# Optimization experiments

Measured on AMD Instinct MI355X. Metric: run time of the kernel, lower is better.

The kernel has to match this reference:

```python
import jax, jax.numpy as jnp
from jax import lax
import numpy as np

N = 131072      # sample_size (number of SDE paths)
T = 500         # number of time points -> T-1 Euler-Maruyama steps
H = 64          # hidden_size of the tiny drift/diffusion MLPs
MU = 0.1
SIGMA = 0.2


def _col_eye(h, scale):
    # emulates scale * eye(h, 1): only [0, 0] element is `scale`
    return jnp.zeros((h, 1), jnp.float32).at[0, 0].set(scale)


def _row_eye(h):
    # emulates eye(1, h): only [0, 0] element is 1
    return jnp.zeros((1, h), jnp.float32).at[0, 0].set(1.0)


def setup_inputs() -> dict:
    key = jax.random.key(0)
    k1, k2 = jax.random.split(key)
    # positive initial prices in [1.0, 1.5) so log(terminal/initial) stays finite
    initial_states = jax.random.uniform(k1, (N, 1), jnp.float32) * 0.5 + 1.0
    times = jnp.linspace(0.0, 1.0, T).astype(jnp.float32)
    # standard-normal draws; scaled by sqrt(dt) inside reference
    noise = jax.random.normal(k2, (T - 1, N, 1), jnp.float32)
    return {
        "initial_states": initial_states,
        "times": times,
        "noise": noise,
        "f1_w": _col_eye(H, MU), "f1_b": jnp.zeros((H,), jnp.float32),
        "f2_w": _row_eye(H),     "f2_b": jnp.zeros((1,), jnp.float32),
        "g1_w": _col_eye(H, SIGMA), "g1_b": jnp.zeros((H,), jnp.float32),
        "g2_w": _row_eye(H),        "g2_b": jnp.zeros((1,), jnp.float32),
    }


def _mlp(y, w1, b1, w2, b2):
    # y: (N, 1) -> (N, 1); tanh(Linear) -> tanh(Linear), as in DeepSDE.f / .g
    h = jnp.tanh(y @ w1.T + b1)          # (N, H)
    return jnp.tanh(h @ w2.T + b2)       # (N, 1)


def reference(initial_states, times, noise,
              f1_w, f1_b, f2_w, f2_b,
              g1_w, g1_b, g2_w, g2_b):
    dts = times[1:] - times[:-1]         # (T-1,)

    def step(y, inp):
        dt, z = inp                      # dt scalar, z (N, 1)
        dW = jnp.sqrt(dt) * z            # Brownian increment
        fv = _mlp(y, f1_w, f1_b, f2_w, f2_b)   # drift, (N, 1)
        gv = _mlp(y, g1_w, g1_b, g2_w, g2_b)   # diffusion (N,1,1) squeezed, brownian_size=1
        return y + fv * dt + gv * dW, None     # Euler-Maruyama (torchsde ito default)

    terminal_states, _ = lax.scan(step, initial_states, (dts, noise))
    return jnp.log(terminal_states / initial_states)  # estimated_log_returns (N, 1)
```

## Files before the change

### kernel.cpp

```cpp
#include <hip/hip_runtime.h>
#include <cstdint>

#define NPATH 131072
#define TPTS  500
#define NSTEP (TPTS - 1)
#define HID   64
#define BLOCK 256

#define K2LOG2E 2.8853900817779268f

__device__ __forceinline__ float fexp2(float x) { return __builtin_amdgcn_exp2f(x); }
__device__ __forceinline__ float frcp(float x)  { return __builtin_amdgcn_rcpf(x); }

__device__ __forceinline__ float sde_step(float y, float dt, float sdt, float z,
                                          float fw1, float fb1, float fw2, float fD,
                                          float gw1, float gb1, float gw2, float gD)
{
    float zdt = sdt * z;
    float ef  = fexp2(fmaf(fw1, y, fb1));
    float rf  = frcp(ef + 1.0f);
    float af  = fmaf(fw2, rf, fD);
    float r2f = frcp(fexp2(af) + 1.0f);
    float fv  = fmaf(-2.0f, r2f, 1.0f);
    float eg  = fexp2(fmaf(gw1, y, gb1));
    float rg  = frcp(eg + 1.0f);
    float ag  = fmaf(gw2, rg, gD);
    float r2g = frcp(fexp2(ag) + 1.0f);
    float gv  = fmaf(-2.0f, r2g, 1.0f);

    y = fmaf(fv, dt, y);
    return fmaf(gv, zdt, y);
}

__global__ __launch_bounds__(BLOCK) void deepsde_kernel(
    const float* __restrict__ y0,
    const float* __restrict__ times,
    const float* __restrict__ noise,
    const float* __restrict__ f1_w, const float* __restrict__ f1_b,
    const float* __restrict__ f2_w, const float* __restrict__ f2_b,
    const float* __restrict__ g1_w, const float* __restrict__ g1_b,
    const float* __restrict__ g2_w, const float* __restrict__ g2_b,
    float* __restrict__ out)
{
    __shared__ float2 s_dt[NSTEP];
    __shared__ float  s_w1p[2][HID], s_b1p[2][HID], s_w2t[2][HID];
    __shared__ float  s_D[2];
    __shared__ int    s_n[2];

    const int tid = threadIdx.x;

    for (int t = tid; t < NSTEP; t += BLOCK) {
        float dt = times[t + 1] - times[t];
        s_dt[t] = make_float2(dt, sqrtf(dt));
    }

    if (tid < 128) {
        const int which = tid >> 6;
        const int lane  = tid & 63;
        const float* w1 = which ? g1_w : f1_w;
        const float* b1 = which ? g1_b : f1_b;
        const float* w2 = which ? g2_w : f2_w;
        const float* b2 = which ? g2_b : f2_b;
        float w1v = w1[lane];
        float b1v = b1[lane];
        float w2v = w2[lane];
        bool active = (w1v != 0.0f);
        unsigned long long mask = __ballot(active);
        float csum = active ? 0.0f : w2v * tanhf(b1v);
        float asum = active ? w2v : 0.0f;
        for (int off = 32; off > 0; off >>= 1) {
            csum += __shfl_down(csum, off);
            asum += __shfl_down(asum, off);
        }
        if (lane == 0) {
            s_n[which] = __popcll(mask);
            s_D[which] = K2LOG2E * (csum + b2[0] + asum);
        }
        if (active) {
            int rank = __popcll(mask & ((1ull << lane) - 1ull));
            s_w1p[which][rank] = K2LOG2E * w1v;
            s_b1p[which][rank] = K2LOG2E * b1v;
            s_w2t[which][rank] = -2.0f * K2LOG2E * w2v;
        }
    }
    __syncthreads();

    const int i = blockIdx.x * BLOCK + tid;
    const int nf = s_n[0], ng = s_n[1];
    const float fD = s_D[0], gD = s_D[1];

    float y = y0[i];
    const float yinit = y;

    if (nf == 1 && ng == 1) {
        const float fw1 = s_w1p[0][0], fb1 = s_b1p[0][0], fw2 = s_w2t[0][0];
        const float gw1 = s_w1p[1][0], gb1 = s_b1p[1][0], gw2 = s_w2t[1][0];

        const float* np = noise + i;

        float z0 = np[0 * NPATH];
        float z1 = np[1 * NPATH];
        float z2 = np[2 * NPATH];
        float z3 = np[3 * NPATH];
        float z4 = np[4 * NPATH];
        float z5 = np[5 * NPATH];
        float z6 = np[6 * NPATH];
        float z7 = np[7 * NPATH];

        int t = 0;
        for (; t + 15 < NSTEP; t += 8) {
            const float* pp = np + (size_t)(t + 8) * NPATH;
            float n0 = pp[0 * NPATH];
            float n1 = pp[1 * NPATH];
            float n2 = pp[2 * NPATH];
            float n3 = pp[3 * NPATH];
            float n4 = pp[4 * NPATH];
            float n5 = pp[5 * NPATH];
            float n6 = pp[6 * NPATH];
            float n7 = pp[7 * NPATH];
            float2 d0 = s_dt[t],     d1 = s_dt[t + 1], d2 = s_dt[t + 2], d3 = s_dt[t + 3];
            float2 d4 = s_dt[t + 4], d5 = s_dt[t + 5], d6 = s_dt[t + 6], d7 = s_dt[t + 7];
            y = sde_step(y, d0.x, d0.y, z0, fw1, fb1, fw2, fD, gw1, gb1, gw2, gD);
            y = sde_step(y, d1.x, d1.y, z1, fw1, fb1, fw2, fD, gw1, gb1, gw2, gD);
            y = sde_step(y, d2.x, d2.y, z2, fw1, fb1, fw2, fD, gw1, gb1, gw2, gD);
            y = sde_step(y, d3.x, d3.y, z3, fw1, fb1, fw2, fD, gw1, gb1, gw2, gD);
            y = sde_step(y, d4.x, d4.y, z4, fw1, fb1, fw2, fD, gw1, gb1, gw2, gD);
            y = sde_step(y, d5.x, d5.y, z5, fw1, fb1, fw2, fD, gw1, gb1, gw2, gD);
            y = sde_step(y, d6.x, d6.y, z6, fw1, fb1, fw2, fD, gw1, gb1, gw2, gD);
            y = sde_step(y, d7.x, d7.y, z7, fw1, fb1, fw2, fD, gw1, gb1, gw2, gD);
            z0 = n0; z1 = n1; z2 = n2; z3 = n3;
            z4 = n4; z5 = n5; z6 = n6; z7 = n7;
        }
        {
            float2 d0 = s_dt[t],     d1 = s_dt[t + 1], d2 = s_dt[t + 2], d3 = s_dt[t + 3];
            float2 d4 = s_dt[t + 4], d5 = s_dt[t + 5], d6 = s_dt[t + 6], d7 = s_dt[t + 7];
            y = sde_step(y, d0.x, d0.y, z0, fw1, fb1, fw2, fD, gw1, gb1, gw2, gD);
            y = sde_step(y, d1.x, d1.y, z1, fw1, fb1, fw2, fD, gw1, gb1, gw2, gD);
            y = sde_step(y, d2.x, d2.y, z2, fw1, fb1, fw2, fD, gw1, gb1, gw2, gD);
            y = sde_step(y, d3.x, d3.y, z3, fw1, fb1, fw2, fD, gw1, gb1, gw2, gD);
            y = sde_step(y, d4.x, d4.y, z4, fw1, fb1, fw2, fD, gw1, gb1, gw2, gD);
            y = sde_step(y, d5.x, d5.y, z5, fw1, fb1, fw2, fD, gw1, gb1, gw2, gD);
            y = sde_step(y, d6.x, d6.y, z6, fw1, fb1, fw2, fD, gw1, gb1, gw2, gD);
            y = sde_step(y, d7.x, d7.y, z7, fw1, fb1, fw2, fD, gw1, gb1, gw2, gD);
        }
        for (t += 8; t < NSTEP; ++t) {
            float z = np[(size_t)t * NPATH];
            float2 d = s_dt[t];
            y = sde_step(y, d.x, d.y, z, fw1, fb1, fw2, fD, gw1, gb1, gw2, gD);
        }
    } else {
        for (int t = 0; t < NSTEP; ++t) {
            float z = noise[(size_t)t * NPATH + i];
            float2 d = s_dt[t];
            float af = fD;
            for (int k = 0; k < nf; ++k) {
                float e = fexp2(fmaf(s_w1p[0][k], y, s_b1p[0][k]));
                float r = frcp(e + 1.0f);
                af = fmaf(s_w2t[0][k], r, af);
            }
            float fv = fmaf(-2.0f, frcp(fexp2(af) + 1.0f), 1.0f);
            float ag = gD;
            for (int k = 0; k < ng; ++k) {
                float e = fexp2(fmaf(s_w1p[1][k], y, s_b1p[1][k]));
                float r = frcp(e + 1.0f);
                ag = fmaf(s_w2t[1][k], r, ag);
            }
            float gv = fmaf(-2.0f, frcp(fexp2(ag) + 1.0f), 1.0f);
            y = fmaf(fv, d.x, y);
            y = fmaf(gv, d.y * z, y);
        }
    }

    out[i] = logf(y / yinit);
}

extern "C" void kernel_launch(void* const* d_in, const int* in_sizes, int n_in,
                              void* d_out, int out_size, void* d_ws, size_t ws_size,
                              hipStream_t stream)
{
    const float* y0    = (const float*)d_in[0];
    const float* times = (const float*)d_in[1];
    const float* noise = (const float*)d_in[2];
    const float* f1_w  = (const float*)d_in[3];
    const float* f1_b  = (const float*)d_in[4];
    const float* f2_w  = (const float*)d_in[5];
    const float* f2_b  = (const float*)d_in[6];
    const float* g1_w  = (const float*)d_in[7];
    const float* g1_b  = (const float*)d_in[8];
    const float* g2_w  = (const float*)d_in[9];
    const float* g2_b  = (const float*)d_in[10];
    float* out = (float*)d_out;

    deepsde_kernel<<<NPATH / BLOCK, BLOCK, 0, stream>>>(
        y0, times, noise,
        f1_w, f1_b, f2_w, f2_b,
        g1_w, g1_b, g2_w, g2_b,
        out);
}
```

Before: 369.8 us.

## Split drift and diffusion MLPs across thread pairs with lane shuffle exchange

Each SDE path is now handled by two adjacent threads: one evaluates the drift MLP and the other the diffusion MLP, and they swap results with a cross-lane shuffle every step. Launching twice as many threads halves the serial transcendental chain per thread, which exposes more parallelism, and launch bounds now request higher occupancy. In exchange both threads load the same noise and dt values and run the same Euler update, and every step adds a shuffle. The kernel was latency-bound with only 512 blocks, so the extra threads are meant to fill the GPU better.

```diff
diff --git a/kernel.cpp b/kernel.cpp
--- a/kernel.cpp
+++ b/kernel.cpp
@@ -6,33 +6,35 @@
 #define NSTEP (TPTS - 1)
 #define HID   64
 #define BLOCK 256
+#define NTHREADS (2 * NPATH)
 
 #define K2LOG2E 2.8853900817779268f
 
 __device__ __forceinline__ float fexp2(float x) { return __builtin_amdgcn_exp2f(x); }
 __device__ __forceinline__ float frcp(float x)  { return __builtin_amdgcn_rcpf(x); }
 
-__device__ __forceinline__ float sde_step(float y, float dt, float sdt, float z,
-                                          float fw1, float fb1, float fw2, float fD,
-                                          float gw1, float gb1, float gw2, float gD)
-{
-    float zdt = sdt * z;
-    float ef  = fexp2(fmaf(fw1, y, fb1));
-    float rf  = frcp(ef + 1.0f);
-    float af  = fmaf(fw2, rf, fD);
-    float r2f = frcp(fexp2(af) + 1.0f);
-    float fv  = fmaf(-2.0f, r2f, 1.0f);
-    float eg  = fexp2(fmaf(gw1, y, gb1));
-    float rg  = frcp(eg + 1.0f);
-    float ag  = fmaf(gw2, rg, gD);
-    float r2g = frcp(fexp2(ag) + 1.0f);
-    float gv  = fmaf(-2.0f, r2g, 1.0f);
-
+__device__ __forceinline__ float mlp1(float y, float w1, float b1, float w2t, float D)
+{
+    float e  = fexp2(fmaf(w1, y, b1));
+    float r  = frcp(e + 1.0f);
+    float a  = fmaf(w2t, r, D);
+    float r2 = frcp(fexp2(a) + 1.0f);
+    return fmaf(-2.0f, r2, 1.0f);
+}
+
+__device__ __forceinline__ float step2(float y, float dt, float sdt, float z, bool role,
+                                       float w1, float b1, float w2t, float D)
+{
+    float zdt    = sdt * z;
+    float mine   = mlp1(y, w1, b1, w2t, D);
+    float theirs = __shfl_xor(mine, 1, 64);
+    float fv = role ? theirs : mine;
+    float gv = role ? mine   : theirs;
     y = fmaf(fv, dt, y);
     return fmaf(gv, zdt, y);
 }
 
-__global__ __launch_bounds__(BLOCK) void deepsde_kernel(
+__global__ __launch_bounds__(BLOCK, 4) void deepsde_kernel(
     const float* __restrict__ y0,
     const float* __restrict__ times,
     const float* __restrict__ noise,
@@ -85,18 +87,22 @@
     }
     __syncthreads();
 
-    const int i = blockIdx.x * BLOCK + tid;
-    const int nf = s_n[0], ng = s_n[1];
-    const float fD = s_D[0], gD = s_D[1];
-
-    float y = y0[i];
+    const bool role = tid & 1;
+    const int  p    = blockIdx.x * (BLOCK / 2) + (tid >> 1);
+    const int  nf = s_n[0], ng = s_n[1];
+
+    float y = y0[p];
     const float yinit = y;
 
     if (nf == 1 && ng == 1) {
-        const float fw1 = s_w1p[0][0], fb1 = s_b1p[0][0], fw2 = s_w2t[0][0];
-        const float gw1 = s_w1p[1][0], gb1 = s_b1p[1][0], gw2 = s_w2t[1][0];
-
-        const float* np = noise + i;
+        const float fw1 = s_w1p[0][0], fb1 = s_b1p[0][0], fw2 = s_w2t[0][0], fDv = s_D[0];
+        const float gw1 = s_w1p[1][0], gb1 = s_b1p[1][0], gw2 = s_w2t[1][0], gDv = s_D[1];
+        const float w1  = role ? gw1 : fw1;
+        const float b1  = role ? gb1 : fb1;
+        const float w2t = role ? gw2 : fw2;
+        const float D   = role ? gDv : fDv;
+
+        const float* np = noise + p;
 
         float z0 = np[0 * NPATH];
         float z1 = np[1 * NPATH];
@@ -120,58 +126,61 @@
             float n7 = pp[7 * NPATH];
             float2 d0 = s_dt[t],     d1 = s_dt[t + 1], d2 = s_dt[t + 2], d3 = s_dt[t + 3];
             float2 d4 = s_dt[t + 4], d5 = s_dt[t + 5], d6 = s_dt[t + 6], d7 = s_dt[t + 7];
-            y = sde_step(y, d0.x, d0.y, z0, fw1, fb1, fw2, fD, gw1, gb1, gw2, gD);
-            y = sde_step(y, d1.x, d1.y, z1, fw1, fb1, fw2, fD, gw1, gb1, gw2, gD);
-            y = sde_step(y, d2.x, d2.y, z2, fw1, fb1, fw2, fD, gw1, gb1, gw2, gD);
-            y = sde_step(y, d3.x, d3.y, z3, fw1, fb1, fw2, fD, gw1, gb1, gw2, gD);
-            y = sde_step(y, d4.x, d4.y, z4, fw1, fb1, fw2, fD, gw1, gb1, gw2, gD);
-            y = sde_step(y, d5.x, d5.y, z5, fw1, fb1, fw2, fD, gw1, gb1, gw2, gD);
-            y = sde_step(y, d6.x, d6.y, z6, fw1, fb1, fw2, fD, gw1, gb1, gw2, gD);
-            y = sde_step(y, d7.x, d7.y, z7, fw1, fb1, fw2, fD, gw1, gb1, gw2, gD);
+            y = step2(y, d0.x, d0.y, z0, role, w1, b1, w2t, D);
+            y = step2(y, d1.x, d1.y, z1, role, w1, b1, w2t, D);
+            y = step2(y, d2.x, d2.y, z2, role, w1, b1, w2t, D);
+            y = step2(y, d3.x, d3.y, z3, role, w1, b1, w2t, D);
+            y = step2(y, d4.x, d4.y, z4, role, w1, b1, w2t, D);
+            y = step2(y, d5.x, d5.y, z5, role, w1, b1, w2t, D);
+            y = step2(y, d6.x, d6.y, z6, role, w1, b1, w2t, D);
+            y = step2(y, d7.x, d7.y, z7, role, w1, b1, w2t, D);
             z0 = n0; z1 = n1; z2 = n2; z3 = n3;
             z4 = n4; z5 = n5; z6 = n6; z7 = n7;
         }
         {
             float2 d0 = s_dt[t],     d1 = s_dt[t + 1], d2 = s_dt[t + 2], d3 = s_dt[t + 3];
             float2 d4 = s_dt[t + 4], d5 = s_dt[t + 5], d6 = s_dt[t + 6], d7 = s_dt[t + 7];
-            y = sde_step(y, d0.x, d0.y, z0, fw1, fb1, fw2, fD, gw1, gb1, gw2, gD);
-            y = sde_step(y, d1.x, d1.y, z1, fw1, fb1, fw2, fD, gw1, gb1, gw2, gD);
-            y = sde_step(y, d2.x, d2.y, z2, fw1, fb1, fw2, fD, gw1, gb1, gw2, gD);
-            y = sde_step(y, d3.x, d3.y, z3, fw1, fb1, fw2, fD, gw1, gb1, gw2, gD);
-            y = sde_step(y, d4.x, d4.y, z4, fw1, fb1, fw2, fD, gw1, gb1, gw2, gD);
-            y = sde_step(y, d5.x, d5.y, z5, fw1, fb1, fw2, fD, gw1, gb1, gw2, gD);
-            y = sde_step(y, d6.x, d6.y, z6, fw1, fb1, fw2, fD, gw1, gb1, gw2, gD);
-            y = sde_step(y, d7.x, d7.y, z7, fw1, fb1, fw2, fD, gw1, gb1, gw2, gD);
+            y = step2(y, d0.x, d0.y, z0, role, w1, b1, w2t, D);
+            y = step2(y, d1.x, d1.y, z1, role, w1, b1, w2t, D);
+            y = step2(y, d2.x, d2.y, z2, role, w1, b1, w2t, D);
+            y = step2(y, d3.x, d3.y, z3, role, w1, b1, w2t, D);
+            y = step2(y, d4.x, d4.y, z4, role, w1, b1, w2t, D);
+            y = step2(y, d5.x, d5.y, z5, role, w1, b1, w2t, D);
+            y = step2(y, d6.x, d6.y, z6, role, w1, b1, w2t, D);
+            y = step2(y, d7.x, d7.y, z7, role, w1, b1, w2t, D);
         }
         for (t += 8; t < NSTEP; ++t) {
             float z = np[(size_t)t * NPATH];
             float2 d = s_dt[t];
-            y = sde_step(y, d.x, d.y, z, fw1, fb1, fw2, fD, gw1, gb1, gw2, gD);
+            y = step2(y, d.x, d.y, z, role, w1, b1, w2t, D);
         }
     } else {
-        for (int t = 0; t < NSTEP; ++t) {
-            float z = noise[(size_t)t * NPATH + i];
-            float2 d = s_dt[t];
-            float af = fD;
-            for (int k = 0; k < nf; ++k) {
-                float e = fexp2(fmaf(s_w1p[0][k], y, s_b1p[0][k]));
-                float r = frcp(e + 1.0f);
-                af = fmaf(s_w2t[0][k], r, af);
+        if (!role) {
+            const float fD = s_D[0], gD = s_D[1];
+            for (int t = 0; t < NSTEP; ++t) {
+                float z = noise[(size_t)t * NPATH + p];
+                float2 d = s_dt[t];
+                float af = fD;
+                for (int k = 0; k < nf; ++k) {
+                    float e = fexp2(fmaf(s_w1p[0][k], y, s_b1p[0][k]));
+                    float r = frcp(e + 1.0f);
+                    af = fmaf(s_w2t[0][k], r, af);
+                }
+                float fv = fmaf(-2.0f, frcp(fexp2(af) + 1.0f), 1.0f);
+                float ag = gD;
+                for (int k = 0; k < ng; ++k) {
+                    float e = fexp2(fmaf(s_w1p[1][k], y, s_b1p[1][k]));
+                    float r = frcp(e + 1.0f);
+                    ag = fmaf(s_w2t[1][k], r, ag);
+                }
+                float gv = fmaf(-2.0f, frcp(fexp2(ag) + 1.0f), 1.0f);
+                y = fmaf(fv, d.x, y);
+                y = fmaf(gv, d.y * z, y);
             }
-            float fv = fmaf(-2.0f, frcp(fexp2(af) + 1.0f), 1.0f);
-            float ag = gD;
-            for (int k = 0; k < ng; ++k) {
-                float e = fexp2(fmaf(s_w1p[1][k], y, s_b1p[1][k]));
-                float r = frcp(e + 1.0f);
-                ag = fmaf(s_w2t[1][k], r, ag);
-            }
-            float gv = fmaf(-2.0f, frcp(fexp2(ag) + 1.0f), 1.0f);
-            y = fmaf(fv, d.x, y);
-            y = fmaf(gv, d.y * z, y);
         }
     }
 
-    out[i] = logf(y / yinit);
+    if (!role) out[p] = logf(y / yinit);
 }
 
 extern "C" void kernel_launch(void* const* d_in, const int* in_sizes, int n_in,
@@ -191,7 +200,7 @@
     const float* g2_b  = (const float*)d_in[10];
     float* out = (float*)d_out;
 
-    deepsde_kernel<<<NPATH / BLOCK, BLOCK, 0, stream>>>(
+    deepsde_kernel<<<NTHREADS / BLOCK, BLOCK, 0, stream>>>(
         y0, times, noise,
         f1_w, f1_b, f2_w, f2_b,
         g1_w, g1_b, g2_w, g2_b,
```

New measurement: 380.4 us. 1.03x slower.
